# Kernel tuning notes

Measured on AMD Instinct MI355X. Metric: run time of the kernel, lower is better.

## Reference

```python
import jax, jax.numpy as jnp
import numpy as np

B, S, D, H = 128, 512, 256, 512
N_ASSETS = 50
OUT_DIM = N_ASSETS * (N_ASSETS + 1) // 2  # 1275, lower-triangular Cholesky entries


def setup_inputs() -> dict:
    key = jax.random.key(0)
    k = jax.random.split(key, 6)
    x = jax.random.normal(k[0], (B, S, D), dtype=jnp.float32)
    # Layer 0: fused gate weights [D+H, 4H] in gate order (i, f, g, o);
    # equivalent to four separate nn.Linear(D+H, H) layers concatenated.
    W0 = jax.random.normal(k[1], (D + H, 4 * H), jnp.float32) / np.sqrt(D + H)
    b0 = jnp.zeros((4 * H,), jnp.float32).at[H:2 * H].set(1.0)  # forget bias = 1.0
    # Layer 1: input is h of layer 0 -> [H+H, 4H]
    W1 = jax.random.normal(k[2], (2 * H, 4 * H), jnp.float32) / np.sqrt(2 * H)
    b1 = jnp.zeros((4 * H,), jnp.float32).at[H:2 * H].set(1.0)
    Wp = jax.random.normal(k[3], (H, OUT_DIM), jnp.float32) / np.sqrt(H)
    bp = jnp.zeros((OUT_DIM,), jnp.float32)
    return {"x": x, "W0": W0, "b0": b0, "W1": W1, "b1": b1, "Wp": Wp, "bp": bp}


def _cell(xt, h, c, W, b):
    # combined = cat(x, h); single fused GEMM for the 4 gates
    z = jnp.concatenate([xt, h], axis=1) @ W + b  # [B, 4H]
    i, f, g, o = jnp.split(z, 4, axis=1)
    c_new = jax.nn.sigmoid(f) * c + jax.nn.sigmoid(i) * jnp.tanh(g)
    h_new = jax.nn.sigmoid(o) * jnp.tanh(c_new)
    return h_new, c_new


def reference(x, W0, b0, W1, b1, Wp, bp):
    batch = x.shape[0]
    hdim = W0.shape[1] // 4
    init = tuple(jnp.zeros((batch, hdim), x.dtype) for _ in range(4))  # h0,c0,h1,c1

    def step(carry, xt):
        h0, c0, h1, c1 = carry
        h0, c0 = _cell(xt, h0, c0, W0, b0)
        h1, c1 = _cell(h0, h1, c1, W1, b1)
        return (h0, c0, h1, c1), None

    (h0, c0, h1, c1), _ = jax.lax.scan(step, init, jnp.swapaxes(x, 0, 1))
    # Original stacks all timestep outputs but only projects the last hidden state.
    return h1 @ Wp + bp  # [B, OUT_DIM]
```

## Files before the change

### kernel.cpp

```cpp
#include <hip/hip_runtime.h>
#include <stdint.h>

#define BATCH 128
#define SEQ   512
#define DIN   256
#define HID   512
#define NWG   256
#define TPB   512
#define NSLOT 513
#define OUTD  1275
#define HSLOT (BATCH * HID)

typedef __attribute__((ext_vector_type(8))) short bf16x8;
typedef __attribute__((ext_vector_type(4))) unsigned int uint4v;
typedef __attribute__((ext_vector_type(4))) float f32x4;

static __device__ __forceinline__ unsigned short f2bf(float f) {
  unsigned int u = __builtin_bit_cast(unsigned int, f);
  u += 0x7FFFu + ((u >> 16) & 1u);
  return (unsigned short)(u >> 16);
}
static __device__ __forceinline__ float sigmoidf_fast(float v) {
  float e = __expf(-fabsf(v));
  float s = 1.0f / (1.0f + e);
  return v >= 0.0f ? s : 1.0f - s;
}
static __device__ __forceinline__ float tanhf_fast(float v) {
  float e = __expf(-2.0f * fabsf(v));
  float t = (1.0f - e) / (1.0f + e);
  return v >= 0.0f ? t : -t;
}

static __device__ __forceinline__ void ldg_nc(bf16x8& d, const unsigned short* p) {
  asm volatile("global_load_dwordx4 %0, %1, off sc0 sc1" : "=v"(d) : "v"(p));
}
static __device__ __forceinline__ void ldg_nc_dw(unsigned int& d, const unsigned int* p) {
  asm volatile("global_load_dword %0, %1, off sc0 sc1" : "=v"(d) : "v"(p));
}
static __device__ __forceinline__ void stg_nc16(unsigned short* p, uint4v v) {
  asm volatile("global_store_dwordx4 %0, %1, off sc0 sc1" :: "v"(p), "v"(v) : "memory");
}
static __device__ __forceinline__ void stg_nc4(unsigned int* p, unsigned int v) {
  asm volatile("global_store_dword %0, %1, off sc0 sc1" :: "v"(p), "v"(v) : "memory");
}
#define WAIT_TIE1(v) asm volatile("s_waitcnt vmcnt(0)" : "+v"(v) :: "memory")
#define WAIT_TIE4(A)                                                          \
  asm volatile("s_waitcnt vmcnt(0)"                                           \
               : "+v"((A)[0]), "+v"((A)[1]), "+v"((A)[2]), "+v"((A)[3])       \
               :: "memory")
#define WAIT_TIE6(A)                                                          \
  asm volatile("s_waitcnt vmcnt(0)"                                           \
               : "+v"((A)[0]), "+v"((A)[1]), "+v"((A)[2]), "+v"((A)[3]),      \
                 "+v"((A)[4]), "+v"((A)[5]) :: "memory")
#define WAIT_TIE8(A)                                                          \
  asm volatile("s_waitcnt vmcnt(0)"                                           \
               : "+v"((A)[0]), "+v"((A)[1]), "+v"((A)[2]), "+v"((A)[3]),      \
                 "+v"((A)[4]), "+v"((A)[5]), "+v"((A)[6]), "+v"((A)[7])       \
               :: "memory")

__global__ __launch_bounds__(256) void xprep(const float* __restrict__ x,
                                             unsigned short* __restrict__ xb) {
  int p = blockIdx.x;
  int lane = threadIdx.x & 63;
  int g4 = threadIdx.x >> 6;
  int c15 = lane & 15, q = lane >> 4;
  for (int g = 0; g < 16; ++g) {
    int idx = g * 4 + g4;
    int mi = idx >> 3, kt = idx & 7;
    int row = mi * 16 + c15;
    const float* src = x + ((size_t)row * SEQ + p) * DIN + kt * 32 + q * 8;
    f32x4 a = *(const f32x4*)src;
    f32x4 b = *(const f32x4*)(src + 4);
    bf16x8 v;
    v[0] = (short)f2bf(a[0]); v[1] = (short)f2bf(a[1]);
    v[2] = (short)f2bf(a[2]); v[3] = (short)f2bf(a[3]);
    v[4] = (short)f2bf(b[0]); v[5] = (short)f2bf(b[1]);
    v[6] = (short)f2bf(b[2]); v[7] = (short)f2bf(b[3]);
    *(bf16x8*)&xb[((((size_t)p * 8 + mi) * 8 + kt) * 64 + lane) * 8] = v;
  }
}

template <bool USE_XB>
__global__ __launch_bounds__(TPB, 1) void lstm_persistent(
    const float* __restrict__ x, const unsigned short* __restrict__ xb,
    const float* __restrict__ W0, const float* __restrict__ b0,
    const float* __restrict__ W1, const float* __restrict__ b1,
    unsigned int* __restrict__ flags, unsigned short* __restrict__ h0buf,
    unsigned short* __restrict__ h1buf, float* __restrict__ h1fin)
{
  __shared__ unsigned short sWf[4 * 32 * 64 * 8];
  __shared__ float red[4 * 32 * 33];
  __shared__ unsigned short stage[32 * 16];

  const int tid  = threadIdx.x;
  const int wgid = blockIdx.x;
  const int g    = wgid >> 6;
  const int r    = wgid & 63;
  const bool isA = (r < 32);
  const int unit0 = (isA ? r : r - 32) << 4;
  const int lane = tid & 63;
  const int wv   = tid >> 6;
  const int m    = wv & 1;
  const int kq   = wv >> 1;
  const int c15  = lane & 15;
  const int q    = lane >> 4;
  const int miG  = g * 2 + m;
  const int KT   = isA ? 24 : 32;

  {
    const float* W = isA ? W0 : W1;
    for (int f = tid; f < 4 * KT * 64; f += TPB) {
      int ct = f / (KT * 64);
      int rem = f - ct * (KT * 64);
      int kt = rem >> 6, ln = rem & 63;
      int qq = ln >> 4, cc = ln & 15;
      int u_local = ct * 4 + (cc >> 2);
      int gate = cc & 3;
      int gcol = gate * HID + unit0 + u_local;
      int kbase = kt * 32 + qq * 8;
      bf16x8 v;
#pragma unroll
      for (int j = 0; j < 8; ++j)
        v[j] = (short)f2bf(W[(size_t)(kbase + j) * 2048 + gcol]);
      *(bf16x8*)&sWf[(size_t)f * 8] = v;
    }
  }

  const int grow_ = tid >> 3, gu = tid & 7;
  float bias_c[2][4];
  float cst[2] = {0.f, 0.f};
  if (tid < 256) {
    const float* bv = isA ? b0 : b1;
#pragma unroll
    for (int ch = 0; ch < 2; ++ch)
#pragma unroll
      for (int gt = 0; gt < 4; ++gt)
        bias_c[ch][gt] = bv[gt * HID + unit0 + ch * 8 + gu];
  }
  __syncthreads();

  unsigned int* myflags = flags + g * 64;

#define BFRAG(ct, kt) (*(const bf16x8*)&sWf[((((ct) * KT + (kt)) << 6) + lane) << 3])

  for (int p = 0; p < NSLOT; ++p) {
    const unsigned short* h0rd = h0buf + ((p + 1) & 1) * HSLOT;
    unsigned short* h0wr       = h0buf + (p & 1) * HSLOT;
    const unsigned short* h1rd = h1buf + (p & 1) * HSLOT;
    unsigned short* h1wr       = h1buf + ((p + 1) & 1) * HSLOT;
    const bool active = isA ? (p < SEQ) : (p >= 1);

    f32x4 acc[4];
#pragma unroll
    for (int ct = 0; ct < 4; ++ct) acc[ct] = (f32x4){0.f, 0.f, 0.f, 0.f};

    if (isA && active) {
      int ktlo = kq * 6, kthi = ktlo + 6;
      for (int kt = ktlo; kt < kthi && kt < 8; ++kt) {
        bf16x8 ax;
        if (USE_XB) {
          ax = *(const bf16x8*)&xb[((((size_t)p * 8 + miG) * 8 + kt) * 64 + lane) * 8];
        } else {
          const float* xp0 = x + (((size_t)(miG * 16 + c15)) * SEQ + p) * DIN + kt * 32 + q * 8;
          f32x4 a = *(const f32x4*)xp0;
          f32x4 b = *(const f32x4*)(xp0 + 4);
          ax[0] = (short)f2bf(a[0]); ax[1] = (short)f2bf(a[1]);
          ax[2] = (short)f2bf(a[2]); ax[3] = (short)f2bf(a[3]);
          ax[4] = (short)f2bf(b[0]); ax[5] = (short)f2bf(b[1]);
          ax[6] = (short)f2bf(b[2]); ax[7] = (short)f2bf(b[3]);
        }
#pragma unroll
        for (int ct = 0; ct < 4; ++ct)
          acc[ct] = __builtin_amdgcn_mfma_f32_16x16x32_bf16(ax, BFRAG(ct, kt), acc[ct], 0, 0, 0);
      }
    }

    if (wv == 0 && p > 0) {
      const unsigned int* fp = myflags + lane;
      for (;;) {
        unsigned int v;
        ldg_nc_dw(v, fp);
        WAIT_TIE1(v);
        if (__ballot(v >= (unsigned int)p) == ~0ull) break;
        __builtin_amdgcn_s_sleep(1);
      }
    }
    __syncthreads();

    if (active) {
      if (isA) {
        if (kq == 1) {
          bf16x8 ah[4];
#pragma unroll
          for (int i = 0; i < 4; ++i)
            ldg_nc(ah[i], h0rd + ((size_t)(miG * 16 + i) * 64 + lane) * 8);
          WAIT_TIE4(ah);
#pragma unroll
          for (int i = 0; i < 4; ++i)
#pragma unroll
            for (int ct = 0; ct < 4; ++ct)
              acc[ct] = __builtin_amdgcn_mfma_f32_16x16x32_bf16(ah[i], BFRAG(ct, 8 + i), acc[ct], 0, 0, 0);
        } else if (kq >= 2) {
          bf16x8 ah[6];
          int kt0 = kq * 6;
#pragma unroll
          for (int i = 0; i < 6; ++i)
            ldg_nc(ah[i], h0rd + ((size_t)(miG * 16 + (kt0 - 8 + i)) * 64 + lane) * 8);
          WAIT_TIE6(ah);
#pragma unroll
          for (int i = 0; i < 6; ++i)
#pragma unroll
            for (int ct = 0; ct < 4; ++ct)
              acc[ct] = __builtin_amdgcn_mfma_f32_16x16x32_bf16(ah[i], BFRAG(ct, kt0 + i), acc[ct], 0, 0, 0);
        }
      } else {
        bf16x8 ah[8];
        const unsigned short* src = (kq < 2) ? h0rd : h1rd;
        int ktf0 = (kq < 2) ? kq * 8 : (kq - 2) * 8;
#pragma unroll
        for (int i = 0; i < 8; ++i)
          ldg_nc(ah[i], src + ((size_t)(miG * 16 + ktf0 + i) * 64 + lane) * 8);
        WAIT_TIE8(ah);
#pragma unroll
        for (int i = 0; i < 8; ++i)
#pragma unroll
          for (int ct = 0; ct < 4; ++ct)
            acc[ct] = __builtin_amdgcn_mfma_f32_16x16x32_bf16(ah[i], BFRAG(ct, kq * 8 + i), acc[ct], 0, 0, 0);
      }
    }

#pragma unroll
    for (int ch = 0; ch < 2; ++ch) {
      __syncthreads();
      if (active) {
        int lrow = m * 16 + q * 4;
#pragma unroll
        for (int t = 0; t < 2; ++t)
#pragma unroll
          for (int rr = 0; rr < 4; ++rr)
            red[(kq * 32 + lrow + rr) * 33 + t * 16 + c15] = acc[ch * 2 + t][rr];
      }
      __syncthreads();
      if (active && tid < 256) {
        float z[4];
#pragma unroll
        for (int gt = 0; gt < 4; ++gt) {
          float s = bias_c[ch][gt];
          int cidx = gu * 4 + gt;
#pragma unroll
          for (int k2 = 0; k2 < 4; ++k2)
            s += red[(k2 * 32 + grow_) * 33 + cidx];
          z[gt] = s;
        }
        float cn = sigmoidf_fast(z[1]) * cst[ch] + sigmoidf_fast(z[0]) * tanhf_fast(z[2]);
        cst[ch] = cn;
        float hn = sigmoidf_fast(z[3]) * tanhf_fast(cn);
        stage[grow_ * 16 + ch * 8 + gu] = f2bf(hn);
        if (!isA && p == NSLOT - 1)
          h1fin[(size_t)(g * 32 + grow_) * HID + unit0 + ch * 8 + gu] = hn;
      }
    }
    __syncthreads();

    if (wv == 0) {
      if (active && tid < 64) {
        int row = tid >> 1, qq2 = tid & 1;
        uint4v v = *(const uint4v*)&stage[row * 16 + qq2 * 8];
        int mi = g * 2 + (row >> 4), r15 = row & 15;
        int ktu = unit0 >> 5;
        int qu = ((unit0 & 31) >> 3) + qq2;
        unsigned short* dst = (isA ? h0wr : h1wr) +
            ((size_t)(mi * 16 + ktu) * 64 + qu * 16 + r15) * 8;
        stg_nc16(dst, v);
      }
      asm volatile("s_waitcnt vmcnt(0)" ::: "memory");
      if (tid == 0) stg_nc4(myflags + r, (unsigned int)(p + 1));
    }
  }
#undef BFRAG
}

__global__ __launch_bounds__(256) void proj_kernel(
    const float* __restrict__ h1, const float* __restrict__ Wp,
    const float* __restrict__ bp, float* __restrict__ out)
{
  int o = blockIdx.x * 256 + threadIdx.x;
  int b = blockIdx.y;
  if (o >= OUTD) return;
  const float* hr = h1 + (size_t)b * HID;
  float acc = bp[o];
#pragma unroll 8
  for (int k = 0; k < HID; ++k)
    acc = fmaf(hr[k], Wp[(size_t)k * OUTD + o], acc);
  out[(size_t)b * OUTD + o] = acc;
}

extern "C" void kernel_launch(void* const* d_in, const int* in_sizes, int n_in,
                              void* d_out, int out_size, void* d_ws, size_t ws_size,
                              hipStream_t stream) {
  const float* x  = (const float*)d_in[0];
  const float* W0 = (const float*)d_in[1];
  const float* b0 = (const float*)d_in[2];
  const float* W1 = (const float*)d_in[3];
  const float* b1 = (const float*)d_in[4];
  const float* Wp = (const float*)d_in[5];
  const float* bp = (const float*)d_in[6];
  float* out = (float*)d_out;

  char* ws = (char*)d_ws;
  unsigned int* flags = (unsigned int*)ws;
  unsigned short* h0b = (unsigned short*)(ws + 4096);
  unsigned short* h1b = (unsigned short*)(ws + 4096 + 262144);
  float* h1fin        = (float*)(ws + 4096 + 2 * 262144);
  unsigned short* xbp = (unsigned short*)(ws + 4096 + 3 * 262144);
  const size_t need_xb = 4096 + 3 * 262144 + (size_t)SEQ * BATCH * DIN * 2;
  const bool use_xb = (ws_size >= need_xb);

  hipMemsetAsync(d_ws, 0, 4096 + 2 * 262144, stream);
  if (use_xb) {
    hipLaunchKernelGGL(xprep, dim3(SEQ), dim3(256), 0, stream, x, xbp);
    hipLaunchKernelGGL(lstm_persistent<true>, dim3(NWG), dim3(TPB), 0, stream,
                       x, xbp, W0, b0, W1, b1, flags, h0b, h1b, h1fin);
  } else {
    hipLaunchKernelGGL(lstm_persistent<false>, dim3(NWG), dim3(TPB), 0, stream,
                       x, xbp, W0, b0, W1, b1, flags, h0b, h1b, h1fin);
  }
  hipLaunchKernelGGL(proj_kernel, dim3((OUTD + 255) / 256, BATCH), dim3(256), 0, stream,
                     h1fin, Wp, bp, out);
}
```

Before: 2.588 ms.

## Decouple layer-0 from layer-1 barrier using a 4-deep h0 ring buffer

Layer-0 workgroups now wait only on the 32 layer-0 flags instead of all 64, and h0 moves from a 2-slot to a 4-slot ring. Before overwriting a slot, layer 0 polls the layer-1 flags to check it is at most two steps ahead. Each poll returns the minimum flag seen, so later steps can skip polling when the dependency is already satisfied. The aim is to let layer 0 run ahead and take the global all-to-all barrier off its critical path, at the cost of more workspace and more involved synchronisation.

```diff
diff --git a/kernel.cpp b/kernel.cpp
--- a/kernel.cpp
+++ b/kernel.cpp
@@ -10,6 +10,13 @@
 #define NSLOT 513
 #define OUTD  1275
 #define HSLOT (BATCH * HID)
+
+#define WS_FLAGS 0
+#define WS_H0    4096
+#define WS_H1    (4096 + 524288)
+#define WS_H1FIN (4096 + 524288 + 262144)
+#define WS_XB    (WS_H1FIN + 262144)
+#define WS_MSET  (4096 + 524288 + 262144)
 
 typedef __attribute__((ext_vector_type(8))) short bf16x8;
 typedef __attribute__((ext_vector_type(4))) unsigned int uint4v;
@@ -57,6 +64,43 @@
                : "+v"((A)[0]), "+v"((A)[1]), "+v"((A)[2]), "+v"((A)[3]),      \
                  "+v"((A)[4]), "+v"((A)[5]), "+v"((A)[6]), "+v"((A)[7])       \
                :: "memory")
+
+static __device__ __forceinline__ int poll_min32(const unsigned int* base, int thr) {
+  const unsigned int* fp = base + (threadIdx.x & 31);
+  for (;;) {
+    unsigned int v;
+    ldg_nc_dw(v, fp);
+    WAIT_TIE1(v);
+    if (__ballot(v >= (unsigned int)thr) == ~0ull) {
+      int mn = (int)v;
+#pragma unroll
+      for (int o = 1; o < 64; o <<= 1) {
+        int t = __shfl_xor(mn, o, 64);
+        mn = t < mn ? t : mn;
+      }
+      return mn;
+    }
+    __builtin_amdgcn_s_sleep(1);
+  }
+}
+static __device__ __forceinline__ int poll_min64(const unsigned int* base, int thr) {
+  const unsigned int* fp = base + (threadIdx.x & 63);
+  for (;;) {
+    unsigned int v;
+    ldg_nc_dw(v, fp);
+    WAIT_TIE1(v);
+    if (__ballot(v >= (unsigned int)thr) == ~0ull) {
+      int mn = (int)v;
+#pragma unroll
+      for (int o = 1; o < 64; o <<= 1) {
+        int t = __shfl_xor(mn, o, 64);
+        mn = t < mn ? t : mn;
+      }
+      return mn;
+    }
+    __builtin_amdgcn_s_sleep(1);
+  }
+}
 
 __global__ __launch_bounds__(256) void xprep(const float* __restrict__ x,
                                              unsigned short* __restrict__ xb) {
@@ -143,11 +187,13 @@
 
 #define BFRAG(ct, kt) (*(const bf16x8*)&sWf[((((ct) * KT + (kt)) << 6) + lane) << 3])
 
+  int selfSeen = 0, bothSeen = 0, ringSeen = 0;
+
   for (int p = 0; p < NSLOT; ++p) {
-    const unsigned short* h0rd = h0buf + ((p + 1) & 1) * HSLOT;
-    unsigned short* h0wr       = h0buf + (p & 1) * HSLOT;
-    const unsigned short* h1rd = h1buf + (p & 1) * HSLOT;
-    unsigned short* h1wr       = h1buf + ((p + 1) & 1) * HSLOT;
+    const unsigned short* h0rd = h0buf + (size_t)((p + 3) & 3) * HSLOT;
+    unsigned short* h0wr       = h0buf + (size_t)(p & 3) * HSLOT;
+    const unsigned short* h1rd = h1buf + (size_t)(p & 1) * HSLOT;
+    unsigned short* h1wr       = h1buf + (size_t)((p + 1) & 1) * HSLOT;
     const bool active = isA ? (p < SEQ) : (p >= 1);
 
     f32x4 acc[4];
@@ -176,13 +222,10 @@
     }
 
     if (wv == 0 && p > 0) {
-      const unsigned int* fp = myflags + lane;
-      for (;;) {
-        unsigned int v;
-        ldg_nc_dw(v, fp);
-        WAIT_TIE1(v);
-        if (__ballot(v >= (unsigned int)p) == ~0ull) break;
-        __builtin_amdgcn_s_sleep(1);
+      if (isA) {
+        if (selfSeen < p) selfSeen = poll_min32(myflags, p);
+      } else {
+        if (bothSeen < p) bothSeen = poll_min64(myflags, p);
       }
     }
     __syncthreads();
@@ -263,6 +306,8 @@
     __syncthreads();
 
     if (wv == 0) {
+      if (isA && active && p > 3 && ringSeen < p - 2)
+        ringSeen = poll_min32(myflags + 32, p - 2);
       if (active && tid < 64) {
         int row = tid >> 1, qq2 = tid & 1;
         uint4v v = *(const uint4v*)&stage[row * 16 + qq2 * 8];
@@ -308,15 +353,15 @@
   float* out = (float*)d_out;
 
   char* ws = (char*)d_ws;
-  unsigned int* flags = (unsigned int*)ws;
-  unsigned short* h0b = (unsigned short*)(ws + 4096);
-  unsigned short* h1b = (unsigned short*)(ws + 4096 + 262144);
-  float* h1fin        = (float*)(ws + 4096 + 2 * 262144);
-  unsigned short* xbp = (unsigned short*)(ws + 4096 + 3 * 262144);
-  const size_t need_xb = 4096 + 3 * 262144 + (size_t)SEQ * BATCH * DIN * 2;
+  unsigned int* flags = (unsigned int*)(ws + WS_FLAGS);
+  unsigned short* h0b = (unsigned short*)(ws + WS_H0);
+  unsigned short* h1b = (unsigned short*)(ws + WS_H1);
+  float* h1fin        = (float*)(ws + WS_H1FIN);
+  unsigned short* xbp = (unsigned short*)(ws + WS_XB);
+  const size_t need_xb = (size_t)WS_XB + (size_t)SEQ * BATCH * DIN * 2;
   const bool use_xb = (ws_size >= need_xb);
 
-  hipMemsetAsync(d_ws, 0, 4096 + 2 * 262144, stream);
+  hipMemsetAsync(d_ws, 0, WS_MSET, stream);
   if (use_xb) {
     hipLaunchKernelGGL(xprep, dim3(SEQ), dim3(256), 0, stream, x, xbp);
     hipLaunchKernelGGL(lstm_persistent<true>, dim3(NWG), dim3(TPB), 0, stream,
```

Result: slower. 2.919 ms (+12.8%).
